# Optimization experiments

Hardware: AMD Instinct MI355X
Metric: run time of the kernel (lower is better)

The kernel has to match this reference:

```python
import jax, jax.numpy as jnp
import numpy as np

N, F, H, D = 4096, 512, 4, 64        # nodes, in features, heads, per-head dim
HID, OUT, NCLS, E = 1024, 256, 40, 65536  # FFN hidden, GAT dim, classes, edges
EPS = 1e-5


def _bn(x, g, b):
    # BatchNorm1d with batch statistics (training-mode math, biased variance)
    m = x.mean(axis=0)
    v = jnp.var(x, axis=0)
    return (x - m) * jax.lax.rsqrt(v + EPS) * g + b


def _ffn(x, g1, b1, W1, c1, g2, b2, W2, c2):
    x = jax.nn.gelu(_bn(x, g1, b1) @ W1.T + c1, approximate=False)
    x = jax.nn.gelu(_bn(x, g2, b2) @ W2.T + c2, approximate=False)
    return x


def setup_inputs() -> dict:
    key = jax.random.key(0)
    ks = jax.random.split(key, 12)
    nrm = lambda k, shape: jax.random.normal(k, shape, jnp.float32) * 0.05
    node_features = jax.random.normal(ks[0], (N, F), jnp.float32)
    edges = jax.random.randint(ks[1], (2, E), 0, N)
    adj = jnp.eye(N, dtype=bool)  # self loops, as in __init__
    adj = adj.at[edges[0], edges[1]].set(True)
    adj = adj.at[edges[1], edges[0]].set(True)
    return dict(
        node_features=node_features,
        pre_g1=jnp.ones(F), pre_b1=jnp.zeros(F),
        pre_W1=nrm(ks[2], (HID, F)), pre_c1=jnp.zeros(HID),
        pre_g2=jnp.ones(HID), pre_b2=jnp.zeros(HID),
        pre_W2=nrm(ks[3], (OUT, HID)), pre_c2=jnp.zeros(OUT),
        Wp=nrm(ks[4], (H * D, OUT)),           # GAT preprocess Linear, no bias
        Wa=nrm(ks[5], (2 * D,)),               # attention Linear(2d -> 1), no bias
        ln_g=jnp.ones(OUT), ln_b=jnp.zeros(OUT),
        post_g1=jnp.ones(OUT), post_b1=jnp.zeros(OUT),
        post_W1=nrm(ks[6], (HID, OUT)), post_c1=jnp.zeros(HID),
        post_g2=jnp.ones(HID), post_b2=jnp.zeros(HID),
        post_W2=nrm(ks[7], (OUT, HID)), post_c2=jnp.zeros(OUT),
        Wl=nrm(ks[8], (NCLS, OUT)), cl=jnp.zeros(NCLS),
        adjacency=adj,
        input_node_indices=jax.random.randint(ks[9], (8192,), 0, N),
    )


def reference(node_features, pre_g1, pre_b1, pre_W1, pre_c1, pre_g2, pre_b2,
              pre_W2, pre_c2, Wp, Wa, ln_g, ln_b, post_g1, post_b1, post_W1,
              post_c1, post_g2, post_b2, post_W2, post_c2, Wl, cl,
              adjacency, input_node_indices):
    # preprocess FFN: [N,F] -> [N,OUT]
    x = _ffn(node_features, pre_g1, pre_b1, pre_W1, pre_c1,
             pre_g2, pre_b2, pre_W2, pre_c2)
    # GAT layer
    xh = (x @ Wp.T).reshape(N, H, D)
    # cat([x_source, x_target]) @ Wa == x[j] . Wa[:D] + x[i] . Wa[D:]
    a_src = jnp.einsum('jhd,d->jh', xh, Wa[:D])
    a_tgt = jnp.einsum('ihd,d->ih', xh, Wa[D:])
    e = jax.nn.leaky_relu(a_src[None, :, :] + a_tgt[:, None, :],
                          negative_slope=0.2)          # [i, j, h]
    e = jnp.where(adjacency[:, :, None], e, -jnp.inf)  # masked_fill(~adj, -inf)
    att = jax.nn.softmax(e, axis=1)                    # softmax over neighbors j
    h = jnp.einsum('ijh,jhd->ihd', att, xh).reshape(N, H * D)
    # residual + LayerNorm (dropout disabled for deterministic reference)
    x = x + h
    mu = x.mean(-1, keepdims=True)
    var = jnp.var(x, axis=-1, keepdims=True)
    x = (x - mu) * jax.lax.rsqrt(var + EPS) * ln_g + ln_b
    # postprocess FFN + gather + logits
    x = _ffn(x, post_g1, post_b1, post_W1, post_c1,
             post_g2, post_b2, post_W2, post_c2)
    emb = x[input_node_indices]
    return emb @ Wl.T + cl
```

## Files before the change

### kernel.cpp

```cpp
#include <hip/hip_runtime.h>
#include <hip/hip_bf16.h>


#define NNODES 4096
#define CAP 128

typedef unsigned short u16;
typedef __attribute__((ext_vector_type(8))) short bf16x8;
typedef __attribute__((ext_vector_type(4))) float f32x4;

__device__ __forceinline__ float gelu_f(float x) {
    return 0.5f * x * (1.0f + erff(x * 0.70710678118654752f));
}
__device__ __forceinline__ u16 f2bf(float x) {
    union { float f; unsigned u; } v; v.f = x;
    unsigned r = v.u + 0x7fff + ((v.u >> 16) & 1);
    return (u16)(r >> 16);
}
__device__ __forceinline__ float bf2f(u16 b) {
    return __uint_as_float(((unsigned)b) << 16);
}
__device__ __forceinline__ void gload16(const void* g, void* l) {
    __builtin_amdgcn_global_load_lds(
        (const __attribute__((address_space(1))) unsigned int*)g,
        (__attribute__((address_space(3))) unsigned int*)l, 16, 0, 0);
}

template<int CPT, bool CVT>
__global__ __launch_bounds__(256) void colstats_partial(
    const float* __restrict__ X, float* __restrict__ part,
    u16* __restrict__ x16, int rpb)
{
    const int C = CPT * 256;
    const int r0 = blockIdx.x * rpb;
    const int t = threadIdx.x;
    float s[CPT], q[CPT];
#pragma unroll
    for (int cc = 0; cc < CPT; ++cc) { s[cc] = 0.f; q[cc] = 0.f; }
    for (int r = 0; r < rpb; ++r) {
        const float* row = X + (size_t)(r0 + r) * C;
#pragma unroll
        for (int cc = 0; cc < CPT; ++cc) {
            float v = row[cc * 256 + t];
            s[cc] += v; q[cc] += v * v;
            if (CVT) x16[(size_t)(r0 + r) * C + cc * 256 + t] = f2bf(v);
        }
    }
#pragma unroll
    for (int cc = 0; cc < CPT; ++cc) {
        int c = cc * 256 + t;
        part[((size_t)blockIdx.x * C + c) * 2 + 0] = s[cc];
        part[((size_t)blockIdx.x * C + c) * 2 + 1] = q[cc];
    }
}

__global__ __launch_bounds__(256) void colstats_final(
    const float* __restrict__ part, const float* __restrict__ g,
    const float* __restrict__ bt, float* __restrict__ scl,
    float* __restrict__ shf, int NB, int C)
{
    __shared__ float sred[16][17];
    __shared__ float qred[16][17];
    const int t = threadIdx.x;
    const int cs = t & 15, grp = t >> 4;
    const int c = blockIdx.x * 16 + cs;
    float s = 0.f, q = 0.f;
    for (int b = grp; b < NB; b += 16) {
        s += part[((size_t)b * C + c) * 2 + 0];
        q += part[((size_t)b * C + c) * 2 + 1];
    }
    sred[grp][cs] = s; qred[grp][cs] = q;
    __syncthreads();
    if (grp == 0) {
        float S = 0.f, Q = 0.f;
#pragma unroll
        for (int j = 0; j < 16; ++j) { S += sred[j][cs]; Q += qred[j][cs]; }
        float m = S * (1.0f / 4096.0f);
        float v = Q * (1.0f / 4096.0f) - m * m;
        float sc = g[c] * rsqrtf(v + 1e-5f);
        scl[c] = sc;
        shf[c] = bt[c] - m * sc;
    }
}

__global__ __launch_bounds__(256) void foldw_kernel(
    const float* __restrict__ W, const float* __restrict__ scl,
    const float* __restrict__ shf, const float* __restrict__ bias,
    u16* __restrict__ W16, float* __restrict__ bout, int K, int nvalid)
{
    __shared__ float red[4];
    const int n = blockIdx.x, t = threadIdx.x;
    u16* o = W16 + (size_t)n * K;
    if (n >= nvalid) {
        for (int k = t; k < K; k += 256) o[k] = 0;
        if (t == 0) bout[n] = 0.f;
        return;
    }
    const float* w = W + (size_t)n * K;
    float part = 0.f;
    for (int k = t; k < K; k += 256) {
        float wv = w[k];
        float s = scl ? scl[k] : 1.f;
        float f = shf ? shf[k] : 0.f;
        o[k] = f2bf(wv * s);
        part += wv * f;
    }
    int lane = t & 63, wv_ = t >> 6;
#pragma unroll
    for (int off = 32; off > 0; off >>= 1) part += __shfl_down(part, off);
    if (lane == 0) red[wv_] = part;
    __syncthreads();
    if (t == 0)
        bout[n] = (bias ? bias[n] : 0.f) + red[0] + red[1] + red[2] + red[3];
}

template<bool EPI, bool S32, bool S16, bool STATS, bool ASRCF>
__global__ __launch_bounds__(256) void mfma_gemm(
    const u16* __restrict__ A, const u16* __restrict__ W,
    const float* __restrict__ bias, float* __restrict__ C32,
    u16* __restrict__ C16, float* __restrict__ PART,
    const float* __restrict__ Wa, float* __restrict__ ASRC,
    float* __restrict__ ATGT, int M, int N, int K)
{
    __shared__ u16 As[2][4096];
    __shared__ u16 Bs[2][4096];
    __shared__ float ep1[2][64];
    __shared__ float ep2[2][64];
    const int t = threadIdx.x;
    const int lane = t & 63, wv = t >> 6;
    const int wm = (wv >> 1) * 32, wn = (wv & 1) * 32;
    const int tile_m = blockIdx.y * 64, tile_n = blockIdx.x * 64;

    f32x4 acc[2][2];
#pragma unroll
    for (int i = 0; i < 2; ++i)
#pragma unroll
        for (int j = 0; j < 2; ++j)
#pragma unroll
            for (int e = 0; e < 4; ++e) acc[i][j][e] = 0.f;

    int srow[2], soff[2];
#pragma unroll
    for (int i = 0; i < 2; ++i) {
        int f = i * 256 + t;
        srow[i] = f >> 3;
        soff[i] = ((f & 7) ^ (srow[i] & 7)) * 8;
    }
    const int wvoff = wv * 1024;
    const int frow_a0 = wm + (lane & 15);
    const int frow_b0 = wn + (lane & 15);
    const int fk = (lane >> 4) * 16;

    const int NT = K >> 6;
    int cur = 0;

#define STAGE(B, KT)                                                        \
    {                                                                        \
        _Pragma("unroll")                                                    \
        for (int i = 0; i < 2; ++i) {                                        \
            gload16(A + (size_t)(tile_m + srow[i]) * K + (KT) * 64 + soff[i],\
                    (char*)As[B] + wvoff + i * 4096);                        \
            gload16(W + (size_t)(tile_n + srow[i]) * K + (KT) * 64 + soff[i],\
                    (char*)Bs[B] + wvoff + i * 4096);                        \
        }                                                                    \
    }

    STAGE(0, 0);
    __syncthreads();
    for (int kt = 0; kt < NT; ++kt) {
        if (kt + 1 < NT) STAGE(cur ^ 1, kt + 1);
        const char* baseA = (const char*)As[cur];
        const char* baseB = (const char*)Bs[cur];
#pragma unroll
        for (int kk = 0; kk < 2; ++kk) {
            bf16x8 a[2], b[2];
#pragma unroll
            for (int mi = 0; mi < 2; ++mi) {
                int r = frow_a0 + mi * 16;
                a[mi] = *(const bf16x8*)(baseA + r * 128 +
                        ((kk * 64 + fk) ^ ((r & 7) << 4)));
            }
#pragma unroll
            for (int ni = 0; ni < 2; ++ni) {
                int r = frow_b0 + ni * 16;
                b[ni] = *(const bf16x8*)(baseB + r * 128 +
                        ((kk * 64 + fk) ^ ((r & 7) << 4)));
            }
#pragma unroll
            for (int mi = 0; mi < 2; ++mi)
#pragma unroll
                for (int ni = 0; ni < 2; ++ni)
                    acc[mi][ni] = __builtin_amdgcn_mfma_f32_16x16x32_bf16(
                        a[mi], b[ni], acc[mi][ni], 0, 0, 0);
        }
        __syncthreads();
        cur ^= 1;
    }
#undef STAGE

    float st0 = 0.f, st1 = 0.f, sq0 = 0.f, sq1 = 0.f;
#pragma unroll
    for (int mi = 0; mi < 2; ++mi) {
#pragma unroll
        for (int ni = 0; ni < 2; ++ni) {
            int col = tile_n + wn + ni * 16 + (lane & 15);
            float bs = 0.f;
            if (EPI) bs = bias[col];
#pragma unroll
            for (int e = 0; e < 4; ++e) {
                int row = tile_m + wm + mi * 16 + ((lane >> 4) << 2) + e;
                float c = acc[mi][ni][e];
                if (EPI) c = gelu_f(c + bs);
                if (S32) C32[(size_t)row * N + col] = c;
                if (S16) C16[(size_t)row * N + col] = f2bf(c);
                if (STATS) {
                    if (ni == 0) { st0 += c; sq0 += c * c; }
                    else         { st1 += c; sq1 += c * c; }
                }
            }
        }
    }

    if (STATS) {
        float s0 = st0, s1 = st1, q0 = sq0, q1 = sq1;
        s0 += __shfl_xor(s0, 16); s0 += __shfl_xor(s0, 32);
        s1 += __shfl_xor(s1, 16); s1 += __shfl_xor(s1, 32);
        q0 += __shfl_xor(q0, 16); q0 += __shfl_xor(q0, 32);
        q1 += __shfl_xor(q1, 16); q1 += __shfl_xor(q1, 32);
        if (lane < 16) {
            ep1[wv >> 1][wn + lane] = s0;       ep2[wv >> 1][wn + lane] = q0;
            ep1[wv >> 1][wn + 16 + lane] = s1;  ep2[wv >> 1][wn + 16 + lane] = q1;
        }
        __syncthreads();
        if (t < 64) {
            float s = ep1[0][t] + ep1[1][t];
            float q = ep2[0][t] + ep2[1][t];
            PART[((size_t)blockIdx.y * N + tile_n + t) * 2 + 0] = s;
            PART[((size_t)blockIdx.y * N + tile_n + t) * 2 + 1] = q;
        }
    }

    if (ASRCF) {
        const int cl = lane & 15;
        float ws0 = Wa[wn + cl],      ws1 = Wa[wn + 16 + cl];
        float wt0 = Wa[64 + wn + cl], wt1 = Wa[64 + wn + 16 + cl];
#pragma unroll
        for (int mi = 0; mi < 2; ++mi)
#pragma unroll
            for (int e = 0; e < 4; ++e) {
                float vs = acc[mi][0][e] * ws0 + acc[mi][1][e] * ws1;
                float vt = acc[mi][0][e] * wt0 + acc[mi][1][e] * wt1;
#pragma unroll
                for (int off = 1; off < 16; off <<= 1) {
                    vs += __shfl_xor(vs, off);
                    vt += __shfl_xor(vt, off);
                }
                if (cl == 0) {
                    int row = wm + mi * 16 + ((lane >> 4) << 2) + e;
                    ep1[wv & 1][row] = vs;
                    ep2[wv & 1][row] = vt;
                }
            }
        __syncthreads();
        if (t < 64) {
            int h = blockIdx.x;
            ASRC[(size_t)(tile_m + t) * 4 + h] = ep1[0][t] + ep1[1][t];
            ATGT[(size_t)(tile_m + t) * 4 + h] = ep2[0][t] + ep2[1][t];
        }
    }
}

__global__ __launch_bounds__(256) void logits_mfma(
    const u16* __restrict__ xf16, const int* __restrict__ idxs,
    const u16* __restrict__ WlP, const float* __restrict__ clP,
    float* __restrict__ out)
{
    __shared__ u16 As[2][4096];
    __shared__ u16 Bs[2][4096];
    const int t = threadIdx.x;
    const int lane = t & 63, wv = t >> 6;
    const int wm = (wv >> 1) * 32, wn = (wv & 1) * 32;
    const int tile_m = blockIdx.x * 64;

    f32x4 acc[2][2];
#pragma unroll
    for (int i = 0; i < 2; ++i)
#pragma unroll
        for (int j = 0; j < 2; ++j)
#pragma unroll
            for (int e = 0; e < 4; ++e) acc[i][j][e] = 0.f;

    int srow[2], soff[2], gr[2];
#pragma unroll
    for (int i = 0; i < 2; ++i) {
        int f = i * 256 + t;
        srow[i] = f >> 3;
        soff[i] = ((f & 7) ^ (srow[i] & 7)) * 8;
        gr[i] = idxs[tile_m + srow[i]];
    }
    const int wvoff = wv * 1024;
    const int frow_a0 = wm + (lane & 15);
    const int frow_b0 = wn + (lane & 15);
    const int fk = (lane >> 4) * 16;

#define LSTAGE(B, KT)                                                       \
    {                                                                        \
        _Pragma("unroll")                                                    \
        for (int i = 0; i < 2; ++i) {                                        \
            gload16(xf16 + (size_t)gr[i] * 256 + (KT) * 64 + soff[i],        \
                    (char*)As[B] + wvoff + i * 4096);                        \
            gload16(WlP + (size_t)srow[i] * 256 + (KT) * 64 + soff[i],       \
                    (char*)Bs[B] + wvoff + i * 4096);                        \
        }                                                                    \
    }

    int cur = 0;
    LSTAGE(0, 0);
    __syncthreads();
#pragma unroll
    for (int kt = 0; kt < 4; ++kt) {
        if (kt + 1 < 4) LSTAGE(cur ^ 1, kt + 1);
        const char* baseA = (const char*)As[cur];
        const char* baseB = (const char*)Bs[cur];
#pragma unroll
        for (int kk = 0; kk < 2; ++kk) {
            bf16x8 a[2], b[2];
#pragma unroll
            for (int mi = 0; mi < 2; ++mi) {
                int r = frow_a0 + mi * 16;
                a[mi] = *(const bf16x8*)(baseA + r * 128 +
                        ((kk * 64 + fk) ^ ((r & 7) << 4)));
            }
#pragma unroll
            for (int ni = 0; ni < 2; ++ni) {
                int r = frow_b0 + ni * 16;
                b[ni] = *(const bf16x8*)(baseB + r * 128 +
                        ((kk * 64 + fk) ^ ((r & 7) << 4)));
            }
#pragma unroll
            for (int mi = 0; mi < 2; ++mi)
#pragma unroll
                for (int ni = 0; ni < 2; ++ni)
                    acc[mi][ni] = __builtin_amdgcn_mfma_f32_16x16x32_bf16(
                        a[mi], b[ni], acc[mi][ni], 0, 0, 0);
        }
        __syncthreads();
        cur ^= 1;
    }
#undef LSTAGE

#pragma unroll
    for (int mi = 0; mi < 2; ++mi) {
#pragma unroll
        for (int ni = 0; ni < 2; ++ni) {
            int col = wn + ni * 16 + (lane & 15);
            if (col < 40) {
                float bs = clP[col];
#pragma unroll
                for (int e = 0; e < 4; ++e) {
                    int row = tile_m + wm + mi * 16 + ((lane >> 4) << 2) + e;
                    out[(size_t)row * 40 + col] = acc[mi][ni][e] + bs;
                }
            }
        }
    }
}

__global__ __launch_bounds__(256) void build_nbr_kernel(
    const unsigned char* __restrict__ adj, int* __restrict__ nbr,
    int* __restrict__ deg)
{
    __shared__ int lists[4][CAP];
    __shared__ int cnts[4];
    __shared__ int sflag;
    const int i = blockIdx.x;
    const int t = threadIdx.x;
    const int wv = t >> 6, lane = t & 63;

    if (wv == 0) {
        bool a = adj[(size_t)lane * 4097] != 0;
        bool b = ((const unsigned int*)adj)[(size_t)lane * 4097] != 0;
        unsigned long long mA = __ballot(a);
        unsigned long long mB = __ballot(b);
        if (lane == 0) sflag = (__popcll(mA) >= __popcll(mB)) ? 0 : 1;
    }
    __syncthreads();
    int cnt = 0;

    if (sflag == 1) {
        const uint4* row = (const uint4*)((const unsigned int*)adj + (size_t)i * NNODES);
#pragma unroll
        for (int w = 0; w < 4; ++w) {
            uint4 v = row[w * 256 + t];
            unsigned wd[4] = {v.x, v.y, v.z, v.w};
#pragma unroll
            for (int j = 0; j < 4; ++j) {
                bool on = wd[j] != 0;
                unsigned long long m = __ballot(on);
                int pre = __popcll(m & ((1ull << lane) - 1ull));
                if (on && cnt + pre < CAP)
                    lists[wv][cnt + pre] = (w * 256 + t) * 4 + j;
                cnt += __popcll(m);
            }
        }
    } else {
        uint4 v = ((const uint4*)(adj + (size_t)i * NNODES))[t];
        unsigned wd[4] = {v.x, v.y, v.z, v.w};
#pragma unroll
        for (int j = 0; j < 4; ++j)
#pragma unroll
            for (int b = 0; b < 4; ++b) {
                bool on = ((wd[j] >> (8 * b)) & 0xffu) != 0;
                unsigned long long m = __ballot(on);
                int pre = __popcll(m & ((1ull << lane) - 1ull));
                if (on && cnt + pre < CAP)
                    lists[wv][cnt + pre] = t * 16 + j * 4 + b;
                cnt += __popcll(m);
            }
    }
    if (lane == 0) cnts[wv] = cnt < CAP ? cnt : CAP;
    __syncthreads();
    int offw = 0;
#pragma unroll
    for (int w2 = 0; w2 < 4; ++w2) if (w2 < wv) offw += cnts[w2];
    int myc = cnts[wv];
    for (int k = lane; k < myc; k += 64) {
        int pos = offw + k;
        if (pos < CAP) nbr[(size_t)i * CAP + pos] = lists[wv][k];
    }
    if (t == 0) {
        int tot = cnts[0] + cnts[1] + cnts[2] + cnts[3];
        deg[i] = tot < CAP ? tot : CAP;
    }
}

__global__ __launch_bounds__(256) void attn_ln_kernel(
    const u16* __restrict__ xh, const float* __restrict__ x0,
    const float* __restrict__ asrc, const float* __restrict__ atgt,
    const int* __restrict__ nbr, const int* __restrict__ deg_,
    const float* __restrict__ ln_g, const float* __restrict__ ln_b,
    float* __restrict__ xln, u16* __restrict__ xln16)
{
    __shared__ float att[CAP * 4];
    __shared__ int nb[CAP];
    __shared__ float red[8];
    const int i = blockIdx.x;
    const int t = threadIdx.x;
    const int dg = deg_[i];

    for (int k = t; k < dg; k += 256) nb[k] = nbr[(size_t)i * CAP + k];
    __syncthreads();

    for (int idx = t; idx < dg * 4; idx += 256) {
        int k = idx >> 2, h = idx & 3;
        float e = asrc[nb[k] * 4 + h] + atgt[i * 4 + h];
        att[idx] = e > 0.f ? e : 0.2f * e;
    }
    __syncthreads();

    const int wv = t >> 6, lane = t & 63;
    {
        const int h = wv;
        float m = -1e30f;
        for (int k = lane; k < dg; k += 64) m = fmaxf(m, att[k * 4 + h]);
#pragma unroll
        for (int off = 32; off > 0; off >>= 1) m = fmaxf(m, __shfl_xor(m, off));
        float s = 0.f;
        for (int k = lane; k < dg; k += 64) s += expf(att[k * 4 + h] - m);
#pragma unroll
        for (int off = 32; off > 0; off >>= 1) s += __shfl_xor(s, off);
        float inv = 1.0f / s;
        for (int k = lane; k < dg; k += 64)
            att[k * 4 + h] = expf(att[k * 4 + h] - m) * inv;
    }
    __syncthreads();

    const int h = t >> 6;
    float acc = 0.f;
    int k = 0;
    for (; k + 4 <= dg; k += 4) {
        float a0 = att[(k + 0) * 4 + h], v0 = bf2f(xh[(size_t)nb[k + 0] * 256 + t]);
        float a1 = att[(k + 1) * 4 + h], v1 = bf2f(xh[(size_t)nb[k + 1] * 256 + t]);
        float a2 = att[(k + 2) * 4 + h], v2 = bf2f(xh[(size_t)nb[k + 2] * 256 + t]);
        float a3 = att[(k + 3) * 4 + h], v3 = bf2f(xh[(size_t)nb[k + 3] * 256 + t]);
        acc = fmaf(a0, v0, acc); acc = fmaf(a1, v1, acc);
        acc = fmaf(a2, v2, acc); acc = fmaf(a3, v3, acc);
    }
    for (; k < dg; ++k)
        acc = fmaf(att[k * 4 + h], bf2f(xh[(size_t)nb[k] * 256 + t]), acc);

    float v = x0[(size_t)i * 256 + t] + acc;
    float s = v, q = v * v;
#pragma unroll
    for (int off = 32; off > 0; off >>= 1) {
        s += __shfl_xor(s, off);
        q += __shfl_xor(q, off);
    }
    if (lane == 0) { red[wv] = s; red[4 + wv] = q; }
    __syncthreads();
    float S = red[0] + red[1] + red[2] + red[3];
    float Q = red[4] + red[5] + red[6] + red[7];
    float mu = S * (1.0f / 256.0f);
    float var = Q * (1.0f / 256.0f) - mu * mu;
    float y = (v - mu) * rsqrtf(var + 1e-5f) * ln_g[t] + ln_b[t];
    xln[(size_t)i * 256 + t] = y;
    xln16[(size_t)i * 256 + t] = f2bf(y);
}

extern "C" void kernel_launch(void* const* d_in, const int* in_sizes, int n_in,
                              void* d_out, int out_size, void* d_ws, size_t ws_size,
                              hipStream_t stream)
{
    const float* nf      = (const float*)d_in[0];
    const float* pre_g1  = (const float*)d_in[1];
    const float* pre_b1  = (const float*)d_in[2];
    const float* pre_W1  = (const float*)d_in[3];
    const float* pre_c1  = (const float*)d_in[4];
    const float* pre_g2  = (const float*)d_in[5];
    const float* pre_b2  = (const float*)d_in[6];
    const float* pre_W2  = (const float*)d_in[7];
    const float* pre_c2  = (const float*)d_in[8];
    const float* Wp      = (const float*)d_in[9];
    const float* Wa      = (const float*)d_in[10];
    const float* ln_g    = (const float*)d_in[11];
    const float* ln_b    = (const float*)d_in[12];
    const float* post_g1 = (const float*)d_in[13];
    const float* post_b1 = (const float*)d_in[14];
    const float* post_W1 = (const float*)d_in[15];
    const float* post_c1 = (const float*)d_in[16];
    const float* post_g2 = (const float*)d_in[17];
    const float* post_b2 = (const float*)d_in[18];
    const float* post_W2 = (const float*)d_in[19];
    const float* post_c2 = (const float*)d_in[20];
    const float* Wl      = (const float*)d_in[21];
    const float* cl      = (const float*)d_in[22];
    const unsigned char* adj = (const unsigned char*)d_in[23];
    const int* idxs      = (const int*)d_in[24];
    float* out = (float*)d_out;

    size_t off = 0;
    char* base = (char*)d_ws;
    auto carve = [&](size_t bytes) {
        void* p = base + off;
        off += (bytes + 255) & ~(size_t)255;
        return p;
    };
    u16*   Y16   = (u16*)  carve((size_t)4096 * 1024 * 2);
    u16*   NF16  = (u16*)  carve((size_t)4096 * 512 * 2);
    float* X032  = (float*)carve((size_t)4096 * 256 * 4);
    u16*   X016  = (u16*)  carve((size_t)4096 * 256 * 2);
    u16*   XH16  = (u16*)  carve((size_t)4096 * 256 * 2);
    float* XLN32 = (float*)carve((size_t)4096 * 256 * 4);
    u16*   XLN16 = (u16*)  carve((size_t)4096 * 256 * 2);
    u16*   XF16  = (u16*)  carve((size_t)4096 * 256 * 2);
    u16*   W1_16 = (u16*)  carve((size_t)1024 * 512 * 2);
    u16*   W2_16 = (u16*)  carve((size_t)256 * 1024 * 2);
    u16*   Wp16  = (u16*)  carve((size_t)256 * 256 * 2);
    u16*   W3_16 = (u16*)  carve((size_t)1024 * 256 * 2);
    u16*   W4_16 = (u16*)  carve((size_t)256 * 1024 * 2);
    u16*   WlP16 = (u16*)  carve((size_t)64 * 256 * 2);
    float* B1    = (float*)carve(1024 * 4);
    float* B2    = (float*)carve(256 * 4);
    float* BP    = (float*)carve(256 * 4);
    float* B3    = (float*)carve(1024 * 4);
    float* B4    = (float*)carve(256 * 4);
    float* CLP   = (float*)carve(64 * 4);
    int*   NBR   = (int*)  carve((size_t)4096 * CAP * 4);
    int*   DEG   = (int*)  carve((size_t)4096 * 4);
    float* ASRC  = (float*)carve((size_t)4096 * 4 * 4);
    float* ATGT  = (float*)carve((size_t)4096 * 4 * 4);
    float* PART  = (float*)carve((size_t)256 * 1024 * 2 * 4);
    float* SCL1  = (float*)carve(512 * 4);
    float* SHF1  = (float*)carve(512 * 4);
    float* SCL2  = (float*)carve(1024 * 4);
    float* SHF2  = (float*)carve(1024 * 4);
    float* SCL3  = (float*)carve(256 * 4);
    float* SHF3  = (float*)carve(256 * 4);
    float* SCL4  = (float*)carve(1024 * 4);
    float* SHF4  = (float*)carve(1024 * 4);
    (void)ws_size; (void)n_in; (void)in_sizes; (void)out_size;

    const int NB = 128, RPB = 4096 / 128;

    build_nbr_kernel<<<4096, 256, 0, stream>>>(adj, NBR, DEG);

    colstats_partial<2, true><<<NB, 256, 0, stream>>>(nf, PART, NF16, RPB);
    colstats_final<<<512 / 16, 256, 0, stream>>>(PART, pre_g1, pre_b1, SCL1, SHF1, NB, 512);
    foldw_kernel<<<1024, 256, 0, stream>>>(pre_W1, SCL1, SHF1, pre_c1, W1_16, B1, 512, 1024);
    mfma_gemm<true, false, true, true, false><<<dim3(16, 64), 256, 0, stream>>>(
        NF16, W1_16, B1, nullptr, Y16, PART, nullptr, nullptr, nullptr,
        4096, 1024, 512);

    colstats_final<<<1024 / 16, 256, 0, stream>>>(PART, pre_g2, pre_b2, SCL2, SHF2, 64, 1024);
    foldw_kernel<<<256, 256, 0, stream>>>(pre_W2, SCL2, SHF2, pre_c2, W2_16, B2, 1024, 256);
    mfma_gemm<true, true, true, false, false><<<dim3(4, 64), 256, 0, stream>>>(
        Y16, W2_16, B2, X032, X016, nullptr, nullptr, nullptr, nullptr,
        4096, 256, 1024);

    foldw_kernel<<<256, 256, 0, stream>>>(Wp, nullptr, nullptr, nullptr, Wp16, BP, 256, 256);
    mfma_gemm<false, false, true, false, true><<<dim3(4, 64), 256, 0, stream>>>(
        X016, Wp16, nullptr, nullptr, XH16, nullptr, Wa, ASRC, ATGT,
        4096, 256, 256);

    attn_ln_kernel<<<4096, 256, 0, stream>>>(XH16, X032, ASRC, ATGT, NBR, DEG,
                                             ln_g, ln_b, XLN32, XLN16);

    colstats_partial<1, false><<<NB, 256, 0, stream>>>(XLN32, PART, nullptr, RPB);
    colstats_final<<<256 / 16, 256, 0, stream>>>(PART, post_g1, post_b1, SCL3, SHF3, NB, 256);
    foldw_kernel<<<1024, 256, 0, stream>>>(post_W1, SCL3, SHF3, post_c1, W3_16, B3, 256, 1024);
    mfma_gemm<true, false, true, true, false><<<dim3(16, 64), 256, 0, stream>>>(
        XLN16, W3_16, B3, nullptr, Y16, PART, nullptr, nullptr, nullptr,
        4096, 1024, 256);

    colstats_final<<<1024 / 16, 256, 0, stream>>>(PART, post_g2, post_b2, SCL4, SHF4, 64, 1024);
    foldw_kernel<<<256, 256, 0, stream>>>(post_W2, SCL4, SHF4, post_c2, W4_16, B4, 1024, 256);
    mfma_gemm<true, false, true, false, false><<<dim3(4, 64), 256, 0, stream>>>(
        Y16, W4_16, B4, nullptr, XF16, nullptr, nullptr, nullptr, nullptr,
        4096, 256, 1024);

    foldw_kernel<<<64, 256, 0, stream>>>(Wl, nullptr, nullptr, cl, WlP16, CLP, 256, 40);
    logits_mfma<<<128, 256, 0, stream>>>(XF16, idxs, WlP16, CLP, out);
}
```

Before: 149.0 us.

## Fuse prep kernels, fold LN column stats into attention, drop fp32 intermediates

```diff
diff --git a/kernel.cpp b/kernel.cpp
--- a/kernel.cpp
+++ b/kernel.cpp
@@ -26,31 +26,97 @@
         (__attribute__((address_space(3))) unsigned int*)l, 16, 0, 0);
 }
 
-template<int CPT, bool CVT>
-__global__ __launch_bounds__(256) void colstats_partial(
-    const float* __restrict__ X, float* __restrict__ part,
-    u16* __restrict__ x16, int rpb)
-{
-    const int C = CPT * 256;
-    const int r0 = blockIdx.x * rpb;
+__global__ __launch_bounds__(256) void prep_kernel(
+    const unsigned char* __restrict__ adj, int* __restrict__ nbr,
+    int* __restrict__ deg, const float* __restrict__ nf,
+    float* __restrict__ part, u16* __restrict__ nf16)
+{
+    __shared__ int lists[4][CAP];
+    __shared__ int cnts[4];
+    __shared__ int sflag;
     const int t = threadIdx.x;
-    float s[CPT], q[CPT];
-#pragma unroll
-    for (int cc = 0; cc < CPT; ++cc) { s[cc] = 0.f; q[cc] = 0.f; }
-    for (int r = 0; r < rpb; ++r) {
-        const float* row = X + (size_t)(r0 + r) * C;
-#pragma unroll
-        for (int cc = 0; cc < CPT; ++cc) {
-            float v = row[cc * 256 + t];
-            s[cc] += v; q[cc] += v * v;
-            if (CVT) x16[(size_t)(r0 + r) * C + cc * 256 + t] = f2bf(v);
-        }
-    }
-#pragma unroll
-    for (int cc = 0; cc < CPT; ++cc) {
-        int c = cc * 256 + t;
-        part[((size_t)blockIdx.x * C + c) * 2 + 0] = s[cc];
-        part[((size_t)blockIdx.x * C + c) * 2 + 1] = q[cc];
+    const int wv = t >> 6, lane = t & 63;
+
+    if (blockIdx.x >= NNODES) {
+        const int bid = blockIdx.x - NNODES;
+        const int r0 = bid * 32;
+        const int cchunk = t & 127;
+        const int rsub = t >> 7;
+        float s[4] = {0.f, 0.f, 0.f, 0.f}, q[4] = {0.f, 0.f, 0.f, 0.f};
+        for (int r = rsub; r < 32; r += 2) {
+            float4 v = *(const float4*)(nf + (size_t)(r0 + r) * 512 + cchunk * 4);
+            float vv[4] = {v.x, v.y, v.z, v.w};
+            ushort4 o;
+            o.x = f2bf(vv[0]); o.y = f2bf(vv[1]);
+            o.z = f2bf(vv[2]); o.w = f2bf(vv[3]);
+            *(ushort4*)(nf16 + (size_t)(r0 + r) * 512 + cchunk * 4) = o;
+#pragma unroll
+            for (int j = 0; j < 4; ++j) { s[j] += vv[j]; q[j] += vv[j] * vv[j]; }
+        }
+        const size_t slice = (size_t)bid * 2 + rsub;
+#pragma unroll
+        for (int j = 0; j < 4; ++j) {
+            int c = cchunk * 4 + j;
+            part[(slice * 512 + c) * 2 + 0] = s[j];
+            part[(slice * 512 + c) * 2 + 1] = q[j];
+        }
+        return;
+    }
+
+    const int i = blockIdx.x;
+    if (wv == 0) {
+        bool a = adj[(size_t)lane * 4097] != 0;
+        bool b = ((const unsigned int*)adj)[(size_t)lane * 4097] != 0;
+        unsigned long long mA = __ballot(a);
+        unsigned long long mB = __ballot(b);
+        if (lane == 0) sflag = (__popcll(mA) >= __popcll(mB)) ? 0 : 1;
+    }
+    __syncthreads();
+    int cnt = 0;
+    if (sflag == 1) {
+        const uint4* row = (const uint4*)((const unsigned int*)adj + (size_t)i * NNODES);
+#pragma unroll
+        for (int w = 0; w < 4; ++w) {
+            uint4 v = row[w * 256 + t];
+            unsigned wd[4] = {v.x, v.y, v.z, v.w};
+#pragma unroll
+            for (int j = 0; j < 4; ++j) {
+                bool on = wd[j] != 0;
+                unsigned long long m = __ballot(on);
+                int pre = __popcll(m & ((1ull << lane) - 1ull));
+                if (on && cnt + pre < CAP)
+                    lists[wv][cnt + pre] = (w * 256 + t) * 4 + j;
+                cnt += __popcll(m);
+            }
+        }
+    } else {
+        uint4 v = ((const uint4*)(adj + (size_t)i * NNODES))[t];
+        unsigned wd[4] = {v.x, v.y, v.z, v.w};
+#pragma unroll
+        for (int j = 0; j < 4; ++j)
+#pragma unroll
+            for (int b = 0; b < 4; ++b) {
+                bool on = ((wd[j] >> (8 * b)) & 0xffu) != 0;
+                unsigned long long m = __ballot(on);
+                int pre = __popcll(m & ((1ull << lane) - 1ull));
+                if (on && cnt + pre < CAP)
+                    lists[wv][cnt + pre] = t * 16 + j * 4 + b;
+                cnt += __popcll(m);
+            }
+    }
+    if (lane == 0) cnts[wv] = cnt < CAP ? cnt : CAP;
+    __syncthreads();
+    int offw = 0;
+#pragma unroll
+    for (int w2 = 0; w2 < 4; ++w2) if (w2 < wv) offw += cnts[w2];
+    int myc = cnts[wv];
+    for (int k = lane; k < myc; k += 64) {
+        int pos = offw + k;
+        if (pos < CAP) nbr[(size_t)i * CAP + pos] = lists[wv][k];
+    }
+    if (t == 0) {
+        int tot = cnts[0] + cnts[1] + cnts[2] + cnts[3];
+        deg[i] = tot < CAP ? tot : CAP;
     }
 }
 
@@ -112,6 +178,26 @@
     __syncthreads();
     if (t == 0)
         bout[n] = (bias ? bias[n] : 0.f) + red[0] + red[1] + red[2] + red[3];
+}
+
+__global__ __launch_bounds__(256) void foldw2_kernel(
+    const float* __restrict__ Wp, const float* __restrict__ Wl,
+    const float* __restrict__ cl, u16* __restrict__ Wp16,
+    u16* __restrict__ WlP16, float* __restrict__ CLP)
+{
+    const int n = blockIdx.x, t = threadIdx.x;
+    if (n < 256) {
+        Wp16[(size_t)n * 256 + t] = f2bf(Wp[(size_t)n * 256 + t]);
+    } else {
+        int m = n - 256;
+        if (m < 40) {
+            WlP16[(size_t)m * 256 + t] = f2bf(Wl[(size_t)m * 256 + t]);
+            if (t == 0) CLP[m] = cl[m];
+        } else {
+            WlP16[(size_t)m * 256 + t] = 0;
+            if (t == 0) CLP[m] = 0.f;
+        }
+    }
 }
 
 template<bool EPI, bool S32, bool S16, bool STATS, bool ASRCF>
@@ -366,145 +452,83 @@
     }
 }
 
-__global__ __launch_bounds__(256) void build_nbr_kernel(
-    const unsigned char* __restrict__ adj, int* __restrict__ nbr,
-    int* __restrict__ deg)
-{
-    __shared__ int lists[4][CAP];
-    __shared__ int cnts[4];
-    __shared__ int sflag;
-    const int i = blockIdx.x;
-    const int t = threadIdx.x;
-    const int wv = t >> 6, lane = t & 63;
-
-    if (wv == 0) {
-        bool a = adj[(size_t)lane * 4097] != 0;
-        bool b = ((const unsigned int*)adj)[(size_t)lane * 4097] != 0;
-        unsigned long long mA = __ballot(a);
-        unsigned long long mB = __ballot(b);
-        if (lane == 0) sflag = (__popcll(mA) >= __popcll(mB)) ? 0 : 1;
-    }
-    __syncthreads();
-    int cnt = 0;
-
-    if (sflag == 1) {
-        const uint4* row = (const uint4*)((const unsigned int*)adj + (size_t)i * NNODES);
-#pragma unroll
-        for (int w = 0; w < 4; ++w) {
-            uint4 v = row[w * 256 + t];
-            unsigned wd[4] = {v.x, v.y, v.z, v.w};
-#pragma unroll
-            for (int j = 0; j < 4; ++j) {
-                bool on = wd[j] != 0;
-                unsigned long long m = __ballot(on);
-                int pre = __popcll(m & ((1ull << lane) - 1ull));
-                if (on && cnt + pre < CAP)
-                    lists[wv][cnt + pre] = (w * 256 + t) * 4 + j;
-                cnt += __popcll(m);
-            }
-        }
-    } else {
-        uint4 v = ((const uint4*)(adj + (size_t)i * NNODES))[t];
-        unsigned wd[4] = {v.x, v.y, v.z, v.w};
-#pragma unroll
-        for (int j = 0; j < 4; ++j)
-#pragma unroll
-            for (int b = 0; b < 4; ++b) {
-                bool on = ((wd[j] >> (8 * b)) & 0xffu) != 0;
-                unsigned long long m = __ballot(on);
-                int pre = __popcll(m & ((1ull << lane) - 1ull));
-                if (on && cnt + pre < CAP)
-                    lists[wv][cnt + pre] = t * 16 + j * 4 + b;
-                cnt += __popcll(m);
-            }
-    }
-    if (lane == 0) cnts[wv] = cnt < CAP ? cnt : CAP;
-    __syncthreads();
-    int offw = 0;
-#pragma unroll
-    for (int w2 = 0; w2 < 4; ++w2) if (w2 < wv) offw += cnts[w2];
-    int myc = cnts[wv];
-    for (int k = lane; k < myc; k += 64) {
-        int pos = offw + k;
-        if (pos < CAP) nbr[(size_t)i * CAP + pos] = lists[wv][k];
-    }
-    if (t == 0) {
-        int tot = cnts[0] + cnts[1] + cnts[2] + cnts[3];
-        deg[i] = tot < CAP ? tot : CAP;
-    }
-}
-
 __global__ __launch_bounds__(256) void attn_ln_kernel(
-    const u16* __restrict__ xh, const float* __restrict__ x0,
+    const u16* __restrict__ xh, const u16* __restrict__ x0,
     const float* __restrict__ asrc, const float* __restrict__ atgt,
     const int* __restrict__ nbr, const int* __restrict__ deg_,
     const float* __restrict__ ln_g, const float* __restrict__ ln_b,
-    float* __restrict__ xln, u16* __restrict__ xln16)
+    u16* __restrict__ xln16, float* __restrict__ PART)
 {
     __shared__ float att[CAP * 4];
     __shared__ int nb[CAP];
     __shared__ float red[8];
-    const int i = blockIdx.x;
     const int t = threadIdx.x;
-    const int dg = deg_[i];
-
-    for (int k = t; k < dg; k += 256) nb[k] = nbr[(size_t)i * CAP + k];
-    __syncthreads();
-
-    for (int idx = t; idx < dg * 4; idx += 256) {
-        int k = idx >> 2, h = idx & 3;
-        float e = asrc[nb[k] * 4 + h] + atgt[i * 4 + h];
-        att[idx] = e > 0.f ? e : 0.2f * e;
-    }
-    __syncthreads();
-
     const int wv = t >> 6, lane = t & 63;
-    {
+    const float g = ln_g[t], bln = ln_b[t];
+    float cs = 0.f, cq = 0.f;
+
+    for (int n = 0; n < 4; ++n) {
+        const int i = blockIdx.x * 4 + n;
+        const int dg = deg_[i];
+        __syncthreads();
+        for (int k = t; k < dg; k += 256) nb[k] = nbr[(size_t)i * CAP + k];
+        __syncthreads();
+
+        for (int idx = t; idx < dg * 4; idx += 256) {
+            int k = idx >> 2, h = idx & 3;
+            float e = asrc[nb[k] * 4 + h] + atgt[i * 4 + h];
+            att[idx] = e > 0.f ? e : 0.2f * e;
+        }
+        __syncthreads();
+
+        {
+            const int h = wv;
+            float m = -1e30f;
+            for (int k = lane; k < dg; k += 64) m = fmaxf(m, att[k * 4 + h]);
+#pragma unroll
+            for (int off = 32; off > 0; off >>= 1) m = fmaxf(m, __shfl_xor(m, off));
+            float s = 0.f;
+            for (int k = lane; k < dg; k += 64) s += expf(att[k * 4 + h] - m);
+#pragma unroll
+            for (int off = 32; off > 0; off >>= 1) s += __shfl_xor(s, off);
+            float inv = 1.0f / s;
+            for (int k = lane; k < dg; k += 64)
+                att[k * 4 + h] = expf(att[k * 4 + h] - m) * inv;
+        }
+
         const int h = wv;
-        float m = -1e30f;
-        for (int k = lane; k < dg; k += 64) m = fmaxf(m, att[k * 4 + h]);
-#pragma unroll
-        for (int off = 32; off > 0; off >>= 1) m = fmaxf(m, __shfl_xor(m, off));
-        float s = 0.f;
-        for (int k = lane; k < dg; k += 64) s += expf(att[k * 4 + h] - m);
-#pragma unroll
-        for (int off = 32; off > 0; off >>= 1) s += __shfl_xor(s, off);
-        float inv = 1.0f / s;
-        for (int k = lane; k < dg; k += 64)
-            att[k * 4 + h] = expf(att[k * 4 + h] - m) * inv;
-    }
-    __syncthreads();
-
-    const int h = t >> 6;
-    float acc = 0.f;
-    int k = 0;
-    for (; k + 4 <= dg; k += 4) {
-        float a0 = att[(k + 0) * 4 + h], v0 = bf2f(xh[(size_t)nb[k + 0] * 256 + t]);
-        float a1 = att[(k + 1) * 4 + h], v1 = bf2f(xh[(size_t)nb[k + 1] * 256 + t]);
-        float a2 = att[(k + 2) * 4 + h], v2 = bf2f(xh[(size_t)nb[k + 2] * 256 + t]);
-        float a3 = att[(k + 3) * 4 + h], v3 = bf2f(xh[(size_t)nb[k + 3] * 256 + t]);
-        acc = fmaf(a0, v0, acc); acc = fmaf(a1, v1, acc);
-        acc = fmaf(a2, v2, acc); acc = fmaf(a3, v3, acc);
-    }
-    for (; k < dg; ++k)
-        acc = fmaf(att[k * 4 + h], bf2f(xh[(size_t)nb[k] * 256 + t]), acc);
-
-    float v = x0[(size_t)i * 256 + t] + acc;
-    float s = v, q = v * v;
-#pragma unroll
-    for (int off = 32; off > 0; off >>= 1) {
-        s += __shfl_xor(s, off);
-        q += __shfl_xor(q, off);
-    }
-    if (lane == 0) { red[wv] = s; red[4 + wv] = q; }
-    __syncthreads();
-    float S = red[0] + red[1] + red[2] + red[3];
-    float Q = red[4] + red[5] + red[6] + red[7];
-    float mu = S * (1.0f / 256.0f);
-    float var = Q * (1.0f / 256.0f) - mu * mu;
-    float y = (v - mu) * rsqrtf(var + 1e-5f) * ln_g[t] + ln_b[t];
-    xln[(size_t)i * 256 + t] = y;
-    xln16[(size_t)i * 256 + t] = f2bf(y);
+        float acc = 0.f;
+        int k = 0;
+        for (; k + 4 <= dg; k += 4) {
+            float a0 = att[(k + 0) * 4 + h], v0 = bf2f(xh[(size_t)nb[k + 0] * 256 + t]);
+            float a1 = att[(k + 1) * 4 + h], v1 = bf2f(xh[(size_t)nb[k + 1] * 256 + t]);
+            float a2 = att[(k + 2) * 4 + h], v2 = bf2f(xh[(size_t)nb[k + 2] * 256 + t]);
+            float a3 = att[(k + 3) * 4 + h], v3 = bf2f(xh[(size_t)nb[k + 3] * 256 + t]);
+            acc = fmaf(a0, v0, acc); acc = fmaf(a1, v1, acc);
+            acc = fmaf(a2, v2, acc); acc = fmaf(a3, v3, acc);
+        }
+        for (; k < dg; ++k)
+            acc = fmaf(att[k * 4 + h], bf2f(xh[(size_t)nb[k] * 256 + t]), acc);
+
+        float v = bf2f(x0[(size_t)i * 256 + t]) + acc;
+        float s = v, q = v * v;
+#pragma unroll
+        for (int off = 32; off > 0; off >>= 1) {
+            s += __shfl_xor(s, off);
+            q += __shfl_xor(q, off);
+        }
+        if (lane == 0) { red[wv] = s; red[4 + wv] = q; }
+        __syncthreads();
+        float S = red[0] + red[1] + red[2] + red[3];
+        float Q = red[4] + red[5] + red[6] + red[7];
+        float mu = S * (1.0f / 256.0f);
+        float var = Q * (1.0f / 256.0f) - mu * mu;
+        float y = (v - mu) * rsqrtf(var + 1e-5f) * g + bln;
+        xln16[(size_t)i * 256 + t] = f2bf(y);
+        cs += y; cq += y * y;
+    }
+    PART[((size_t)blockIdx.x * 256 + t) * 2 + 0] = cs;
+    PART[((size_t)blockIdx.x * 256 + t) * 2 + 1] = cq;
 }
 
 extern "C" void kernel_launch(void* const* d_in, const int* in_sizes, int n_in,
@@ -547,10 +571,8 @@
     };
     u16*   Y16   = (u16*)  carve((size_t)4096 * 1024 * 2);
     u16*   NF16  = (u16*)  carve((size_t)4096 * 512 * 2);
-    float* X032  = (float*)carve((size_t)4096 * 256 * 4);
     u16*   X016  = (u16*)  carve((size_t)4096 * 256 * 2);
     u16*   XH16  = (u16*)  carve((size_t)4096 * 256 * 2);
-    float* XLN32 = (float*)carve((size_t)4096 * 256 * 4);
     u16*   XLN16 = (u16*)  carve((size_t)4096 * 256 * 2);
     u16*   XF16  = (u16*)  carve((size_t)4096 * 256 * 2);
     u16*   W1_16 = (u16*)  carve((size_t)1024 * 512 * 2);
@@ -561,7 +583,6 @@
     u16*   WlP16 = (u16*)  carve((size_t)64 * 256 * 2);
     float* B1    = (float*)carve(1024 * 4);
     float* B2    = (float*)carve(256 * 4);
-    float* BP    = (float*)carve(256 * 4);
     float* B3    = (float*)carve(1024 * 4);
     float* B4    = (float*)carve(256 * 4);
     float* CLP   = (float*)carve(64 * 4);
@@ -569,7 +590,7 @@
     int*   DEG   = (int*)  carve((size_t)4096 * 4);
     float* ASRC  = (float*)carve((size_t)4096 * 4 * 4);
     float* ATGT  = (float*)carve((size_t)4096 * 4 * 4);
-    float* PART  = (float*)carve((size_t)256 * 1024 * 2 * 4);
+    float* PART  = (float*)carve((size_t)1024 * 512 * 2 * 4);
     float* SCL1  = (float*)carve(512 * 4);
     float* SHF1  = (float*)carve(512 * 4);
     float* SCL2  = (float*)carve(1024 * 4);
@@ -580,12 +601,9 @@
     float* SHF4  = (float*)carve(1024 * 4);
     (void)ws_size; (void)n_in; (void)in_sizes; (void)out_size;
 
-    const int NB = 128, RPB = 4096 / 128;
-
-    build_nbr_kernel<<<4096, 256, 0, stream>>>(adj, NBR, DEG);
-
-    colstats_partial<2, true><<<NB, 256, 0, stream>>>(nf, PART, NF16, RPB);
-    colstats_final<<<512 / 16, 256, 0, stream>>>(PART, pre_g1, pre_b1, SCL1, SHF1, NB, 512);
+    prep_kernel<<<NNODES + 128, 256, 0, stream>>>(adj, NBR, DEG, nf, PART, NF16);
+
+    colstats_final<<<512 / 16, 256, 0, stream>>>(PART, pre_g1, pre_b1, SCL1, SHF1, 256, 512);
     foldw_kernel<<<1024, 256, 0, stream>>>(pre_W1, SCL1, SHF1, pre_c1, W1_16, B1, 512, 1024);
     mfma_gemm<true, false, true, true, false><<<dim3(16, 64), 256, 0, stream>>>(
         NF16, W1_16, B1, nullptr, Y16, PART, nullptr, nullptr, nullptr,
@@ -593,20 +611,20 @@
 
     colstats_final<<<1024 / 16, 256, 0, stream>>>(PART, pre_g2, pre_b2, SCL2, SHF2, 64, 1024);
     foldw_kernel<<<256, 256, 0, stream>>>(pre_W2, SCL2, SHF2, pre_c2, W2_16, B2, 1024, 256);
-    mfma_gemm<true, true, true, false, false><<<dim3(4, 64), 256, 0, stream>>>(
-        Y16, W2_16, B2, X032, X016, nullptr, nullptr, nullptr, nullptr,
+    mfma_gemm<true, false, true, false, false><<<dim3(4, 64), 256, 0, stream>>>(
+        Y16, W2_16, B2, nullptr, X016, nullptr, nullptr, nullptr, nullptr,
         4096, 256, 1024);
 
-    foldw_kernel<<<256, 256, 0, stream>>>(Wp, nullptr, nullptr, nullptr, Wp16, BP, 256, 256);
+    foldw2_kernel<<<320, 256, 0, stream>>>(Wp, Wl, cl, Wp16, WlP16, CLP);
+
     mfma_gemm<false, false, true, false, true><<<dim3(4, 64), 256, 0, stream>>>(
         X016, Wp16, nullptr, nullptr, XH16, nullptr, Wa, ASRC, ATGT,
         4096, 256, 256);
 
-    attn_ln_kernel<<<4096, 256, 0, stream>>>(XH16, X032, ASRC, ATGT, NBR, DEG,
-                                             ln_g, ln_b, XLN32, XLN16);
-
-    colstats_partial<1, false><<<NB, 256, 0, stream>>>(XLN32, PART, nullptr, RPB);
-    colstats_final<<<256 / 16, 256, 0, stream>>>(PART, post_g1, post_b1, SCL3, SHF3, NB, 256);
+    attn_ln_kernel<<<1024, 256, 0, stream>>>(XH16, X016, ASRC, ATGT, NBR, DEG,
+                                             ln_g, ln_b, XLN16, PART);
+
+    colstats_final<<<256 / 16, 256, 0, stream>>>(PART, post_g1, post_b1, SCL3, SHF3, 1024, 256);
     foldw_kernel<<<1024, 256, 0, stream>>>(post_W1, SCL3, SHF3, post_c1, W3_16, B3, 256, 1024);
     mfma_gemm<true, false, true, true, false><<<dim3(16, 64), 256, 0, stream>>>(
         XLN16, W3_16, B3, nullptr, Y16, PART, nullptr, nullptr, nullptr,
@@ -618,6 +636,5 @@
         Y16, W4_16, B4, nullptr, XF16, nullptr, nullptr, nullptr, nullptr,
         4096, 256, 1024);
 
-    foldw_kernel<<<64, 256, 0, stream>>>(Wl, nullptr, nullptr, cl, WlP16, CLP, 256, 40);
     logits_mfma<<<128, 256, 0, stream>>>(XF16, idxs, WlP16, CLP, out);
 }
```

New measurement: 156.8 us. 1.05x slower.
